# Kernel tuning notes

Hardware: AMD Instinct MI355X
Metric: run time of the kernel (lower is better)

Reference implementation:

```python
import jax, jax.numpy as jnp
import numpy as np

N = 25000; E = 100000; H = 64; NODE_IN = 32; EDGE_IN = 16; L = 3


def _lin(key, fan_in, fan_out):
    kw, kb = jax.random.split(key)
    s = 1.0 / np.sqrt(fan_in)
    W = jax.random.uniform(kw, (fan_out, fan_in), minval=-s, maxval=s, dtype=jnp.float32)
    b = jax.random.uniform(kb, (fan_out,), minval=-s, maxval=s, dtype=jnp.float32)
    return W, b


def setup_inputs() -> dict:
    key = jax.random.key(0)
    ks = jax.random.split(key, 16)
    x = jax.random.normal(ks[0], (N, NODE_IN), dtype=jnp.float32)
    edge_attr = jax.random.normal(ks[1], (E, EDGE_IN), dtype=jnp.float32)
    edge_index = jax.random.randint(ks[2], (2, E), 0, N, dtype=jnp.int32)
    Wn1, bn1 = _lin(ks[3], NODE_IN, H)
    Wn2, bn2 = _lin(ks[4], H, H)
    Wn3, bn3 = _lin(ks[5], H, H)
    We1, be1 = _lin(ks[6], EDGE_IN, H)
    We2, be2 = _lin(ks[7], H, H)
    We3, be3 = _lin(ks[8], H, H * H)
    roots = jax.random.normal(ks[9], (L, H, H), dtype=jnp.float32) / np.sqrt(H)
    conv_bias = jnp.zeros((L, H), dtype=jnp.float32)
    s = 1.0 / np.sqrt(H)
    gru_Wih = jax.random.uniform(ks[10], (3 * H, H), minval=-s, maxval=s, dtype=jnp.float32)
    gru_Whh = jax.random.uniform(ks[11], (3 * H, H), minval=-s, maxval=s, dtype=jnp.float32)
    gru_bih = jax.random.uniform(ks[12], (3 * H,), minval=-s, maxval=s, dtype=jnp.float32)
    gru_bhh = jax.random.uniform(ks[13], (3 * H,), minval=-s, maxval=s, dtype=jnp.float32)
    return dict(x=x, edge_attr=edge_attr,
                Wn1=Wn1, bn1=bn1, Wn2=Wn2, bn2=bn2, Wn3=Wn3, bn3=bn3,
                We1=We1, be1=be1, We2=We2, be2=be2, We3=We3, be3=be3,
                roots=roots, conv_bias=conv_bias,
                gru_Wih=gru_Wih, gru_Whh=gru_Whh, gru_bih=gru_bih, gru_bhh=gru_bhh,
                edge_index=edge_index)


def _mpnn_forward(x, edge_attr, Wn1, bn1, Wn2, bn2, Wn3, bn3,
                  We1, be1, We2, be2, We3, be3,
                  roots, conv_bias, gru_Wih, gru_Whh, gru_bih, gru_bhh, edge_index):
    src, dst = edge_index[0], edge_index[1]
    # mlp_in: Linear-ReLU-Linear-ReLU-Linear
    h = jax.nn.relu(x @ Wn1.T + bn1)
    h = jax.nn.relu(h @ Wn2.T + bn2)
    h = h @ Wn3.T + bn3  # [N, H]
    # edge MLP is shared across all NNConv layers and edge_attr is constant -> compute once
    ew = jax.nn.relu(edge_attr @ We1.T + be1)
    ew = jax.nn.relu(ew @ We2.T + be2)
    ew = (ew @ We3.T + be3).reshape(E, H, H)  # per-edge weight [E, in, out]
    hidden = jnp.zeros((x.shape[0], H), dtype=h.dtype)  # GRU hidden (1 layer)
    for l in range(L):
        # NNConv: message_e = h[src_e] @ W_e, scatter-add to dst, plus root term and bias
        msg = jnp.einsum('ei,eio->eo', h[src], ew)
        aggr = jax.ops.segment_sum(msg, dst, num_segments=N)
        m = aggr + h @ roots[l] + conv_bias[l]  # [N, H]
        # GRU step (seq_len=1, batch=N)
        gi = m @ gru_Wih.T + gru_bih
        gh = hidden @ gru_Whh.T + gru_bhh
        i_r, i_z, i_n = jnp.split(gi, 3, axis=-1)
        h_r, h_z, h_n = jnp.split(gh, 3, axis=-1)
        r = jax.nn.sigmoid(i_r + h_r)
        z = jax.nn.sigmoid(i_z + h_z)
        n = jnp.tanh(i_n + r * h_n)
        hidden = (1.0 - z) * n + z * hidden
        h = hidden  # output of 1-layer GRU == new hidden
    return h


def reference(x, edge_attr, Wn1, bn1, Wn2, bn2, Wn3, bn3,
              We1, be1, We2, be2, We3, be3,
              roots, conv_bias, gru_Wih, gru_Whh, gru_bih, gru_bhh, edge_index):
    return _mpnn_forward(x, edge_attr, Wn1, bn1, Wn2, bn2, Wn3, bn3,
                         We1, be1, We2, be2, We3, be3,
                         roots, conv_bias, gru_Wih, gru_Whh, gru_bih, gru_bhh, edge_index)
```

## Files before the change

### kernel.cpp

```cpp
#include <hip/hip_runtime.h>
#include <math.h>

#define NN 25000
#define NE 100000

typedef _Float16 f16;
typedef _Float16 half8 __attribute__((ext_vector_type(8)));
typedef float f32x4 __attribute__((ext_vector_type(4)));

__global__ __launch_bounds__(256) void prep_all(
    const float* __restrict__ Wn1, const float* __restrict__ Wn2,
    const float* __restrict__ Wn3, const float* __restrict__ We1,
    const float* __restrict__ We2, const float* __restrict__ Wih,
    const float* __restrict__ Whh, const float* __restrict__ We3,
    const float* __restrict__ be3, const float* __restrict__ roots,
    float* __restrict__ T, f16* __restrict__ Wf16, f16* __restrict__ root16,
    f16* __restrict__ Wih16, f16* __restrict__ Whh16)
{
    int f = blockIdx.x * 256 + threadIdx.x;
    if (f >= 318464) return;
    if (f < 15360) {
        if (f < 2048)       { int j = f;         T[f] = Wn1[(j & 63) * 32 + (j >> 6)]; }
        else if (f < 6144)  { int j = f - 2048;  T[f] = Wn2[(j & 63) * 64 + (j >> 6)]; }
        else if (f < 10240) { int j = f - 6144;  T[f] = Wn3[(j & 63) * 64 + (j >> 6)]; }
        else if (f < 11264) { int j = f - 10240; T[f] = We1[(j & 63) * 16 + (j >> 6)]; }
        else                { int j = f - 11264; T[f] = We2[(j & 63) * 64 + (j >> 6)]; }
    } else {
        int g = f - 15360;
        if (g < 266240) {
            if (g < 262144) Wf16[g] = (f16)We3[g];
            else {
                int j = g - 262144; int o = (j >> 6), k = j & 63;
                Wf16[g] = (f16)be3[k * 64 + o];
            }
        } else {
            int g2 = g - 266240;
            if (g2 < 12288) {
                int l = g2 >> 12, j = g2 & 4095, o = j >> 6, i = j & 63;
                root16[g2] = (f16)roots[l * 4096 + i * 64 + o];
            } else if (g2 < 24576) Wih16[g2 - 12288] = (f16)Wih[g2 - 12288];
            else                   Whh16[g2 - 24576] = (f16)Whh[g2 - 24576];
        }
    }
}

__global__ __launch_bounds__(256) void node_mlp(
    const float* __restrict__ x, const float* __restrict__ T,
    const float* __restrict__ bn1, const float* __restrict__ bn2,
    const float* __restrict__ bn3,
    float* __restrict__ hbuf, f16* __restrict__ h16, float* __restrict__ aggr)
{
    __shared__ float sx[4][8][32];
    __shared__ float sh1[4][8][64];
    const float* Wn1T = T;
    const float* Wn2T = T + 2048;
    const float* Wn3T = T + 6144;
    int w = threadIdx.x >> 6, lane = threadIdx.x & 63;
    int n0 = blockIdx.x * 32 + w * 8;
    if (n0 >= NN) return;
    #pragma unroll
    for (int jj = 0; jj < 4; ++jj) {
        int f = jj * 64 + lane;
        sx[w][f >> 5][f & 31] = x[(size_t)(n0 + (f >> 5)) * 32 + (f & 31)];
    }
    float a[8];
    #pragma unroll
    for (int j = 0; j < 8; ++j) a[j] = bn1[lane];
    for (int i = 0; i < 32; i += 4) {
        float4 bb[8];
        #pragma unroll
        for (int j = 0; j < 8; ++j) bb[j] = *(const float4*)&sx[w][j][i];
        #pragma unroll
        for (int ii = 0; ii < 4; ++ii) {
            float wv = Wn1T[(i + ii) * 64 + lane];
            #pragma unroll
            for (int j = 0; j < 8; ++j) a[j] += ((const float*)&bb[j])[ii] * wv;
        }
    }
    #pragma unroll
    for (int j = 0; j < 8; ++j) { sh1[w][j][lane] = fmaxf(a[j], 0.f); a[j] = bn2[lane]; }
    for (int i = 0; i < 64; i += 4) {
        float4 bb[8];
        #pragma unroll
        for (int j = 0; j < 8; ++j) bb[j] = *(const float4*)&sh1[w][j][i];
        #pragma unroll
        for (int ii = 0; ii < 4; ++ii) {
            float wv = Wn2T[(i + ii) * 64 + lane];
            #pragma unroll
            for (int j = 0; j < 8; ++j) a[j] += ((const float*)&bb[j])[ii] * wv;
        }
    }
    #pragma unroll
    for (int j = 0; j < 8; ++j) { sh1[w][j][lane] = fmaxf(a[j], 0.f); a[j] = bn3[lane]; }
    for (int i = 0; i < 64; i += 4) {
        float4 bb[8];
        #pragma unroll
        for (int j = 0; j < 8; ++j) bb[j] = *(const float4*)&sh1[w][j][i];
        #pragma unroll
        for (int ii = 0; ii < 4; ++ii) {
            float wv = Wn3T[(i + ii) * 64 + lane];
            #pragma unroll
            for (int j = 0; j < 8; ++j) a[j] += ((const float*)&bb[j])[ii] * wv;
        }
    }
    #pragma unroll
    for (int j = 0; j < 8; ++j) {
        size_t idx = (size_t)(n0 + j) * 64 + lane;
        hbuf[idx] = a[j];
        h16[idx]  = (f16)a[j];
        aggr[idx] = 0.f;
    }
}

__global__ __launch_bounds__(256) void edge_mlp(
    const float* __restrict__ ea, const float* __restrict__ T,
    const float* __restrict__ be1, const float* __restrict__ be2,
    f16* __restrict__ ew16)
{
    __shared__ float sa[4][8][16];
    __shared__ float st[4][8][64];
    const float* We1T = T + 10240;
    const float* We2T = T + 11264;
    int w = threadIdx.x >> 6, lane = threadIdx.x & 63;
    int e0 = blockIdx.x * 32 + w * 8;
    if (e0 >= NE) return;
    #pragma unroll
    for (int jj = 0; jj < 2; ++jj) {
        int f = jj * 64 + lane;
        sa[w][f >> 4][f & 15] = ea[(size_t)(e0 + (f >> 4)) * 16 + (f & 15)];
    }
    float a[8];
    #pragma unroll
    for (int j = 0; j < 8; ++j) a[j] = be1[lane];
    for (int i = 0; i < 16; i += 4) {
        float4 bb[8];
        #pragma unroll
        for (int j = 0; j < 8; ++j) bb[j] = *(const float4*)&sa[w][j][i];
        #pragma unroll
        for (int ii = 0; ii < 4; ++ii) {
            float wv = We1T[(i + ii) * 64 + lane];
            #pragma unroll
            for (int j = 0; j < 8; ++j) a[j] += ((const float*)&bb[j])[ii] * wv;
        }
    }
    #pragma unroll
    for (int j = 0; j < 8; ++j) { st[w][j][lane] = fmaxf(a[j], 0.f); a[j] = be2[lane]; }
    for (int i = 0; i < 64; i += 4) {
        float4 bb[8];
        #pragma unroll
        for (int j = 0; j < 8; ++j) bb[j] = *(const float4*)&st[w][j][i];
        #pragma unroll
        for (int ii = 0; ii < 4; ++ii) {
            float wv = We2T[(i + ii) * 64 + lane];
            #pragma unroll
            for (int j = 0; j < 8; ++j) a[j] += ((const float*)&bb[j])[ii] * wv;
        }
    }
    #pragma unroll
    for (int j = 0; j < 8; ++j)
        ew16[(size_t)(e0 + j) * 64 + lane] = (f16)fmaxf(a[j], 0.f);
}

__device__ __forceinline__ half8 splat8(f16 v)
{ half8 r = { v, v, v, v, v, v, v, v }; return r; }

__device__ __forceinline__ void mfma_block(
    const char* bb, int swzA, int swzB,
    half8 aA0, half8 aA1, half8 aB0, half8 aB1, f32x4 (&acc)[2][4])
{
    half8 b00 = *(const half8*)(bb + 0    + swzA);
    half8 b01 = *(const half8*)(bb + 0    + swzB);
    half8 b10 = *(const half8*)(bb + 2048 + swzA);
    half8 b11 = *(const half8*)(bb + 2048 + swzB);
    half8 b20 = *(const half8*)(bb + 4096 + swzA);
    half8 b21 = *(const half8*)(bb + 4096 + swzB);
    half8 b30 = *(const half8*)(bb + 6144 + swzA);
    half8 b31 = *(const half8*)(bb + 6144 + swzB);
    acc[0][0] = __builtin_amdgcn_mfma_f32_16x16x32_f16(aA0, b00, acc[0][0], 0, 0, 0);
    acc[0][0] = __builtin_amdgcn_mfma_f32_16x16x32_f16(aA1, b01, acc[0][0], 0, 0, 0);
    acc[0][1] = __builtin_amdgcn_mfma_f32_16x16x32_f16(aA0, b10, acc[0][1], 0, 0, 0);
    acc[0][1] = __builtin_amdgcn_mfma_f32_16x16x32_f16(aA1, b11, acc[0][1], 0, 0, 0);
    acc[0][2] = __builtin_amdgcn_mfma_f32_16x16x32_f16(aA0, b20, acc[0][2], 0, 0, 0);
    acc[0][2] = __builtin_amdgcn_mfma_f32_16x16x32_f16(aA1, b21, acc[0][2], 0, 0, 0);
    acc[0][3] = __builtin_amdgcn_mfma_f32_16x16x32_f16(aA0, b30, acc[0][3], 0, 0, 0);
    acc[0][3] = __builtin_amdgcn_mfma_f32_16x16x32_f16(aA1, b31, acc[0][3], 0, 0, 0);
    acc[1][0] = __builtin_amdgcn_mfma_f32_16x16x32_f16(aB0, b00, acc[1][0], 0, 0, 0);
    acc[1][0] = __builtin_amdgcn_mfma_f32_16x16x32_f16(aB1, b01, acc[1][0], 0, 0, 0);
    acc[1][1] = __builtin_amdgcn_mfma_f32_16x16x32_f16(aB0, b10, acc[1][1], 0, 0, 0);
    acc[1][1] = __builtin_amdgcn_mfma_f32_16x16x32_f16(aB1, b11, acc[1][1], 0, 0, 0);
    acc[1][2] = __builtin_amdgcn_mfma_f32_16x16x32_f16(aB0, b20, acc[1][2], 0, 0, 0);
    acc[1][2] = __builtin_amdgcn_mfma_f32_16x16x32_f16(aB1, b21, acc[1][2], 0, 0, 0);
    acc[1][3] = __builtin_amdgcn_mfma_f32_16x16x32_f16(aB0, b30, acc[1][3], 0, 0, 0);
    acc[1][3] = __builtin_amdgcn_mfma_f32_16x16x32_f16(aB1, b31, acc[1][3], 0, 0, 0);
}

__global__ __launch_bounds__(256) void msg_mfma(
    const f16* __restrict__ h16, const f16* __restrict__ ew16,
    const f16* __restrict__ Wf16, const int* __restrict__ edge_index,
    float* __restrict__ aggr)
{
    __shared__ f16 sh_h[128][72];
    __shared__ f16 sh_ring[4][4096];
    __shared__ int sh_dst[128];
    int t = threadIdx.x, lane = t & 63, wv = t >> 6;
    int e0 = blockIdx.x * 128;
    char* ringc = (char*)&sh_ring[0][0];

    const uint4* gW = (const uint4*)Wf16;
    uint4 r0 = gW[t], r1 = gW[256 + t], r2 = gW[512 + t], r3 = gW[768 + t];

    {
        int row = t >> 1, part = t & 1;
        int e = e0 + row;
        bool valid = e < NE;
        int ec = valid ? e : NE - 1;
        int src = edge_index[ec];
        const uint4* hp = (const uint4*)(h16 + (size_t)src * 64 + part * 32);
        const uint4* ep = (const uint4*)(ew16 + (size_t)ec * 64 + part * 32);
        uint4 z = make_uint4(0u, 0u, 0u, 0u);
        uint4 h0 = hp[0], h1 = hp[1], h2 = hp[2], h3 = hp[3];
        uint4 g0 = valid ? ep[0] : z;
        uint4 g1 = valid ? ep[1] : z;
        uint4 g2 = valid ? ep[2] : z;
        uint4 g3 = valid ? ep[3] : z;
        *(uint4*)&sh_h[row][part * 32]      = h0;
        *(uint4*)&sh_h[row][part * 32 + 8]  = h1;
        *(uint4*)&sh_h[row][part * 32 + 16] = h2;
        *(uint4*)&sh_h[row][part * 32 + 24] = h3;
        int rb = row * 128, key = (row & 7) << 4;
        *(uint4*)(ringc + rb + ((part * 64 +  0) ^ key)) = g0;
        *(uint4*)(ringc + rb + ((part * 64 + 16) ^ key)) = g1;
        *(uint4*)(ringc + rb + ((part * 64 + 32) ^ key)) = g2;
        *(uint4*)(ringc + rb + ((part * 64 + 48) ^ key)) = g3;
        if (lane < 32) {
            int e2 = e0 + wv * 32 + lane;
            sh_dst[wv * 32 + lane] = (e2 < NE) ? edge_index[NE + e2] : -1;
        }
    }

    int r16 = lane & 15, kq = lane >> 4;
    int row0 = wv * 32 + r16, row1 = row0 + 16;

    int k0 = (row0 & 7) << 4, k1 = (row1 & 7) << 4;
    half8 evA0 = *(const half8*)(ringc + row0 * 128 + ((kq * 16) ^ k0));
    half8 evA1 = *(const half8*)(ringc + row0 * 128 + ((64 + kq * 16) ^ k0));
    half8 evB0 = *(const half8*)(ringc + row1 * 128 + ((kq * 16) ^ k1));
    half8 evB1 = *(const half8*)(ringc + row1 * 128 + ((64 + kq * 16) ^ k1));

    __syncthreads();

    int d0 = t * 16, d1 = 4096 + t * 16;
    int dsw0 = d0 ^ (((d0 >> 7) & 7) << 4);
    int dsw1 = d1 ^ (((d1 >> 7) & 7) << 4);

    *(uint4*)(ringc + dsw0) = r0;
    *(uint4*)(ringc + dsw1) = r1;
    *(uint4*)(ringc + 8192 + dsw0) = r2;
    *(uint4*)(ringc + 8192 + dsw1) = r3;
    r0 = gW[2 * 512 + t]; r1 = gW[2 * 512 + 256 + t];
    r2 = gW[3 * 512 + t]; r3 = gW[3 * 512 + 256 + t];
    __syncthreads();

    f32x4 acc[2][4];
    #pragma unroll
    for (int m = 0; m < 2; ++m)
        #pragma unroll
        for (int n = 0; n < 4; ++n) acc[m][n] = (f32x4){0, 0, 0, 0};

    int swzA = (kq << 4) ^ ((r16 & 7) << 4);
    int swzB = ((kq << 4) | 64) ^ ((r16 & 7) << 4);

    for (int i8 = 0; i8 < 8; ++i8) {
        half8 hA = *(const half8*)&sh_h[row0][i8 * 8];
        half8 hB = *(const half8*)&sh_h[row1][i8 * 8];
        #pragma unroll
        for (int w2 = 0; w2 < 4; ++w2) {
            const char* pairR = ringc + (w2 & 1) * 16384 + r16 * 128;
            #pragma unroll
            for (int s = 0; s < 2; ++s) {
                f16 hsA = hA[w2 * 2 + s];
                f16 hsB = hB[w2 * 2 + s];
                mfma_block(pairR + s * 8192, swzA, swzB,
                           evA0 * splat8(hsA), evA1 * splat8(hsA),
                           evB0 * splat8(hsB), evB1 * splat8(hsB), acc);
            }
            char* wb = ringc + ((w2 + 1) & 1) * 16384;
            *(uint4*)(wb + dsw0) = r0;
            *(uint4*)(wb + dsw1) = r1;
            *(uint4*)(wb + 8192 + dsw0) = r2;
            *(uint4*)(wb + 8192 + dsw1) = r3;
            int jw = i8 * 4 + w2;
            int sA = jw * 2 + 4; if (sA > 64) sA = 64;
            int sB = jw * 2 + 5; if (sB > 64) sB = 64;
            r0 = gW[(size_t)sA * 512 + t]; r1 = gW[(size_t)sA * 512 + 256 + t];
            r2 = gW[(size_t)sB * 512 + t]; r3 = gW[(size_t)sB * 512 + 256 + t];
            __syncthreads();
        }
    }

    {
        const char* bb = ringc + r16 * 128;
        half8 aA0 = *(const half8*)&sh_h[row0][kq * 8];
        half8 aA1 = *(const half8*)&sh_h[row0][32 + kq * 8];
        half8 aB0 = *(const half8*)&sh_h[row1][kq * 8];
        half8 aB1 = *(const half8*)&sh_h[row1][32 + kq * 8];
        mfma_block(bb, swzA, swzB, aA0, aA1, aB0, aB1, acc);
    }

    #pragma unroll
    for (int m = 0; m < 2; ++m) {
        #pragma unroll
        for (int reg = 0; reg < 4; ++reg) {
            int e_l = wv * 32 + m * 16 + kq * 4 + reg;
            int d = sh_dst[e_l];
            if (d >= 0) {
                float* ap = aggr + (size_t)d * 64 + r16;
                atomicAdd(ap,      acc[m][0][reg]);
                atomicAdd(ap + 16, acc[m][1][reg]);
                atomicAdd(ap + 32, acc[m][2][reg]);
                atomicAdd(ap + 48, acc[m][3][reg]);
            }
        }
    }
}

__global__ __launch_bounds__(256) void gru_mfma(
    float* __restrict__ aggr, float* __restrict__ hbuf, f16* __restrict__ h16,
    const f16* __restrict__ root16, const float* __restrict__ cbias,
    const f16* __restrict__ Wih16, const f16* __restrict__ Whh16,
    const float* __restrict__ bih, const float* __restrict__ bhh,
    float* __restrict__ out2, int first)
{
    __shared__ f16 sh[64][72];
    __shared__ f16 sm[64][72];
    int t = threadIdx.x, lane = t & 63, wv = t >> 6;
    int n0 = blockIdx.x * 64;

    {
        int row = t >> 2, part = t & 3;
        int n = n0 + row;
        uint4 z = make_uint4(0u, 0u, 0u, 0u);
        const uint4* hp = (const uint4*)(h16 + (size_t)n * 64 + part * 16);
        uint4 v0 = (n < NN) ? hp[0] : z;
        uint4 v1 = (n < NN) ? hp[1] : z;
        *(uint4*)&sh[row][part * 16]     = v0;
        *(uint4*)&sh[row][part * 16 + 8] = v1;
    }
    __syncthreads();

    int r16 = lane & 15, kq = lane >> 4;
    int wr = wv * 16;
    int rowA = wr + r16;
    half8 ah0 = *(const half8*)&sh[rowA][kq * 8];
    half8 ah1 = *(const half8*)&sh[rowA][32 + kq * 8];
    int nodeBase = wr + kq * 4;

    f32x4 accm[4];
    #pragma unroll
    for (int tt = 0; tt < 4; ++tt) {
        int o = tt * 16 + r16;
        float cb = cbias[o];
        #pragma unroll
        for (int reg = 0; reg < 4; ++reg) {
            int n = n0 + nodeBase + reg;
            float v = 0.f;
            if (n < NN) {
                size_t ix = (size_t)n * 64 + o;
                v = aggr[ix] + cb;
                aggr[ix] = 0.f;
            }
            accm[tt][reg] = v;
        }
    }
    #pragma unroll
    for (int tt = 0; tt < 4; ++tt) {
        const f16* bp = root16 + (size_t)(tt * 16 + r16) * 64 + kq * 8;
        half8 b0 = *(const half8*)bp;
        half8 b1 = *(const half8*)(bp + 32);
        accm[tt] = __builtin_amdgcn_mfma_f32_16x16x32_f16(ah0, b0, accm[tt], 0, 0, 0);
        accm[tt] = __builtin_amdgcn_mfma_f32_16x16x32_f16(ah1, b1, accm[tt], 0, 0, 0);
    }
    #pragma unroll
    for (int tt = 0; tt < 4; ++tt)
        #pragma unroll
        for (int reg = 0; reg < 4; ++reg)
            sm[nodeBase + reg][tt * 16 + r16] = (f16)accm[tt][reg];
    __syncthreads();
    half8 am0 = *(const half8*)&sm[rowA][kq * 8];
    half8 am1 = *(const half8*)&sm[rowA][32 + kq * 8];

    f32x4 acc_rz[8], acc_in[4], acc_hn[4];
    #pragma unroll
    for (int tt = 0; tt < 8; ++tt) acc_rz[tt] = (f32x4){0, 0, 0, 0};
    #pragma unroll
    for (int tt = 0; tt < 4; ++tt) { acc_in[tt] = (f32x4){0, 0, 0, 0}; acc_hn[tt] = (f32x4){0, 0, 0, 0}; }

    #pragma unroll
    for (int tt = 0; tt < 8; ++tt) {
        const f16* bp = Wih16 + (size_t)(tt * 16 + r16) * 64 + kq * 8;
        half8 b0 = *(const half8*)bp;
        half8 b1 = *(const half8*)(bp + 32);
        acc_rz[tt] = __builtin_amdgcn_mfma_f32_16x16x32_f16(am0, b0, acc_rz[tt], 0, 0, 0);
        acc_rz[tt] = __builtin_amdgcn_mfma_f32_16x16x32_f16(am1, b1, acc_rz[tt], 0, 0, 0);
    }
    #pragma unroll
    for (int tt = 0; tt < 4; ++tt) {
        const f16* bp = Wih16 + (size_t)(128 + tt * 16 + r16) * 64 + kq * 8;
        half8 b0 = *(const half8*)bp;
        half8 b1 = *(const half8*)(bp + 32);
        acc_in[tt] = __builtin_amdgcn_mfma_f32_16x16x32_f16(am0, b0, acc_in[tt], 0, 0, 0);
        acc_in[tt] = __builtin_amdgcn_mfma_f32_16x16x32_f16(am1, b1, acc_in[tt], 0, 0, 0);
    }
    if (!first) {
        #pragma unroll
        for (int tt = 0; tt < 8; ++tt) {
            const f16* bp = Whh16 + (size_t)(tt * 16 + r16) * 64 + kq * 8;
            half8 b0 = *(const half8*)bp;
            half8 b1 = *(const half8*)(bp + 32);
            acc_rz[tt] = __builtin_amdgcn_mfma_f32_16x16x32_f16(ah0, b0, acc_rz[tt], 0, 0, 0);
            acc_rz[tt] = __builtin_amdgcn_mfma_f32_16x16x32_f16(ah1, b1, acc_rz[tt], 0, 0, 0);
        }
        #pragma unroll
        for (int tt = 0; tt < 4; ++tt) {
            const f16* bp = Whh16 + (size_t)(128 + tt * 16 + r16) * 64 + kq * 8;
            half8 b0 = *(const half8*)bp;
            half8 b1 = *(const half8*)(bp + 32);
            acc_hn[tt] = __builtin_amdgcn_mfma_f32_16x16x32_f16(ah0, b0, acc_hn[tt], 0, 0, 0);
            acc_hn[tt] = __builtin_amdgcn_mfma_f32_16x16x32_f16(ah1, b1, acc_hn[tt], 0, 0, 0);
        }
    }

    #pragma unroll
    for (int tt = 0; tt < 4; ++tt) {
        int o = tt * 16 + r16;
        float b_r = bih[o] + bhh[o];
        float b_z = bih[64 + o] + bhh[64 + o];
        float bin = bih[128 + o];
        float bhn = bhh[128 + o];
        #pragma unroll
        for (int reg = 0; reg < 4; ++reg) {
            int n = n0 + nodeBase + reg;
            if (n >= NN) continue;
            size_t ix = (size_t)n * 64 + o;
            float rv = 1.f / (1.f + expf(-(acc_rz[tt][reg] + b_r)));
            float zv = 1.f / (1.f + expf(-(acc_rz[4 + tt][reg] + b_z)));
            float hn_ = first ? bhn : (acc_hn[tt][reg] + bhn);
            float nv = tanhf(acc_in[tt][reg] + bin + rv * hn_);
            float hold = first ? 0.f : hbuf[ix];
            float outv = (1.f - zv) * nv + zv * hold;
            hbuf[ix] = outv;
            h16[ix]  = (f16)outv;
            if (out2) out2[ix] = outv;
        }
    }
}

extern "C" void kernel_launch(void* const* d_in, const int* in_sizes, int n_in,
                              void* d_out, int out_size, void* d_ws, size_t ws_size,
                              hipStream_t stream)
{
    const float* x   = (const float*)d_in[0];
    const float* ea  = (const float*)d_in[1];
    const float* Wn1 = (const float*)d_in[2];  const float* bn1 = (const float*)d_in[3];
    const float* Wn2 = (const float*)d_in[4];  const float* bn2 = (const float*)d_in[5];
    const float* Wn3 = (const float*)d_in[6];  const float* bn3 = (const float*)d_in[7];
    const float* We1 = (const float*)d_in[8];  const float* be1 = (const float*)d_in[9];
    const float* We2 = (const float*)d_in[10]; const float* be2 = (const float*)d_in[11];
    const float* We3 = (const float*)d_in[12]; const float* be3 = (const float*)d_in[13];
    const float* roots = (const float*)d_in[14];
    const float* cb    = (const float*)d_in[15];
    const float* Wih = (const float*)d_in[16]; const float* Whh = (const float*)d_in[17];
    const float* bih = (const float*)d_in[18]; const float* bhh = (const float*)d_in[19];
    const int*   ei  = (const int*)d_in[20];

    float* ws   = (float*)d_ws;
    float* hbuf = ws;
    float* aggr = hbuf + (size_t)NN * 64;
    float* Tbuf = aggr + (size_t)NN * 64;
    f16*   h16  = (f16*)(ws + 2 * (size_t)NN * 64 + 16384);
    f16*   ew16 = h16  + (size_t)NN * 64;
    f16*   Wf16 = ew16 + (size_t)NE * 64;
    f16*   root16 = Wf16 + 266240;
    f16*   Wih16  = root16 + 12288;
    f16*   Whh16  = Wih16 + 12288;

    prep_all<<<(318464 + 255) / 256, 256, 0, stream>>>(Wn1, Wn2, Wn3, We1, We2,
        Wih, Whh, We3, be3, roots, Tbuf, Wf16, root16, Wih16, Whh16);
    node_mlp<<<(NN + 31) / 32, 256, 0, stream>>>(x, Tbuf, bn1, bn2, bn3,
                                                 hbuf, h16, aggr);
    edge_mlp<<<NE / 32, 256, 0, stream>>>(ea, Tbuf, be1, be2, ew16);

    for (int l = 0; l < 3; ++l) {
        msg_mfma<<<(NE + 127) / 128, 256, 0, stream>>>(h16, ew16, Wf16, ei, aggr);
        gru_mfma<<<(NN + 63) / 64, 256, 0, stream>>>(aggr, hbuf, h16,
            root16 + (size_t)l * 4096, cb + (size_t)l * 64,
            Wih16, Whh16, bih, bhh,
            (l == 2) ? (float*)d_out : nullptr, (l == 0) ? 1 : 0);
    }
}
```

Baseline: 409.4 us.

## Split msg MFMA work by output column per wave; shrink GRU blocks to one wave

The message kernel now assigns each wave a 16-column slice of the output across all 128 edges, instead of 32 edges across all 64 columns. Each B fragment of the per-edge weight is then loaded once and reused across eight M-tiles, which cuts LDS reads per MFMA but holds 16 edge vectors in registers and scales them per tile. It also adds a barrier before the edge loads. The GRU kernel becomes a single-wave 64-thread block over 16 nodes, dropping its __syncthreads; this gives more, smaller blocks and relies on in-wave ordering for the shared-memory exchange.

```diff
diff --git a/kernel.cpp b/kernel.cpp
--- a/kernel.cpp
+++ b/kernel.cpp
@@ -163,36 +163,6 @@
 
 __device__ __forceinline__ half8 splat8(f16 v)
 { half8 r = { v, v, v, v, v, v, v, v }; return r; }
-
-__device__ __forceinline__ void mfma_block(
-    const char* bb, int swzA, int swzB,
-    half8 aA0, half8 aA1, half8 aB0, half8 aB1, f32x4 (&acc)[2][4])
-{
-    half8 b00 = *(const half8*)(bb + 0    + swzA);
-    half8 b01 = *(const half8*)(bb + 0    + swzB);
-    half8 b10 = *(const half8*)(bb + 2048 + swzA);
-    half8 b11 = *(const half8*)(bb + 2048 + swzB);
-    half8 b20 = *(const half8*)(bb + 4096 + swzA);
-    half8 b21 = *(const half8*)(bb + 4096 + swzB);
-    half8 b30 = *(const half8*)(bb + 6144 + swzA);
-    half8 b31 = *(const half8*)(bb + 6144 + swzB);
-    acc[0][0] = __builtin_amdgcn_mfma_f32_16x16x32_f16(aA0, b00, acc[0][0], 0, 0, 0);
-    acc[0][0] = __builtin_amdgcn_mfma_f32_16x16x32_f16(aA1, b01, acc[0][0], 0, 0, 0);
-    acc[0][1] = __builtin_amdgcn_mfma_f32_16x16x32_f16(aA0, b10, acc[0][1], 0, 0, 0);
-    acc[0][1] = __builtin_amdgcn_mfma_f32_16x16x32_f16(aA1, b11, acc[0][1], 0, 0, 0);
-    acc[0][2] = __builtin_amdgcn_mfma_f32_16x16x32_f16(aA0, b20, acc[0][2], 0, 0, 0);
-    acc[0][2] = __builtin_amdgcn_mfma_f32_16x16x32_f16(aA1, b21, acc[0][2], 0, 0, 0);
-    acc[0][3] = __builtin_amdgcn_mfma_f32_16x16x32_f16(aA0, b30, acc[0][3], 0, 0, 0);
-    acc[0][3] = __builtin_amdgcn_mfma_f32_16x16x32_f16(aA1, b31, acc[0][3], 0, 0, 0);
-    acc[1][0] = __builtin_amdgcn_mfma_f32_16x16x32_f16(aB0, b00, acc[1][0], 0, 0, 0);
-    acc[1][0] = __builtin_amdgcn_mfma_f32_16x16x32_f16(aB1, b01, acc[1][0], 0, 0, 0);
-    acc[1][1] = __builtin_amdgcn_mfma_f32_16x16x32_f16(aB0, b10, acc[1][1], 0, 0, 0);
-    acc[1][1] = __builtin_amdgcn_mfma_f32_16x16x32_f16(aB1, b11, acc[1][1], 0, 0, 0);
-    acc[1][2] = __builtin_amdgcn_mfma_f32_16x16x32_f16(aB0, b20, acc[1][2], 0, 0, 0);
-    acc[1][2] = __builtin_amdgcn_mfma_f32_16x16x32_f16(aB1, b21, acc[1][2], 0, 0, 0);
-    acc[1][3] = __builtin_amdgcn_mfma_f32_16x16x32_f16(aB0, b30, acc[1][3], 0, 0, 0);
-    acc[1][3] = __builtin_amdgcn_mfma_f32_16x16x32_f16(aB1, b31, acc[1][3], 0, 0, 0);
-}
 
 __global__ __launch_bounds__(256) void msg_mfma(
     const f16* __restrict__ h16, const f16* __restrict__ ew16,
@@ -237,15 +207,20 @@
             sh_dst[wv * 32 + lane] = (e2 < NE) ? edge_index[NE + e2] : -1;
         }
     }
+    __syncthreads();
 
     int r16 = lane & 15, kq = lane >> 4;
-    int row0 = wv * 32 + r16, row1 = row0 + 16;
-
-    int k0 = (row0 & 7) << 4, k1 = (row1 & 7) << 4;
-    half8 evA0 = *(const half8*)(ringc + row0 * 128 + ((kq * 16) ^ k0));
-    half8 evA1 = *(const half8*)(ringc + row0 * 128 + ((64 + kq * 16) ^ k0));
-    half8 evB0 = *(const half8*)(ringc + row1 * 128 + ((kq * 16) ^ k1));
-    half8 evB1 = *(const half8*)(ringc + row1 * 128 + ((64 + kq * 16) ^ k1));
+
+    half8 ev0[8], ev1[8];
+    {
+        int key = (r16 & 7) << 4;
+        #pragma unroll
+        for (int m = 0; m < 8; ++m) {
+            int row = m * 16 + r16;
+            ev0[m] = *(const half8*)(ringc + row * 128 + ((kq * 16) ^ key));
+            ev1[m] = *(const half8*)(ringc + row * 128 + ((64 + kq * 16) ^ key));
+        }
+    }
 
     __syncthreads();
 
@@ -261,28 +236,35 @@
     r2 = gW[3 * 512 + t]; r3 = gW[3 * 512 + 256 + t];
     __syncthreads();
 
-    f32x4 acc[2][4];
-    #pragma unroll
-    for (int m = 0; m < 2; ++m)
-        #pragma unroll
-        for (int n = 0; n < 4; ++n) acc[m][n] = (f32x4){0, 0, 0, 0};
+    f32x4 acc[8];
+    #pragma unroll
+    for (int m = 0; m < 8; ++m) acc[m] = (f32x4){0, 0, 0, 0};
 
     int swzA = (kq << 4) ^ ((r16 & 7) << 4);
     int swzB = ((kq << 4) | 64) ^ ((r16 & 7) << 4);
+    int colBase = wv * 2048 + r16 * 128;
 
     for (int i8 = 0; i8 < 8; ++i8) {
-        half8 hA = *(const half8*)&sh_h[row0][i8 * 8];
-        half8 hB = *(const half8*)&sh_h[row1][i8 * 8];
+        half8 hM[8];
+        #pragma unroll
+        for (int m = 0; m < 8; ++m)
+            hM[m] = *(const half8*)&sh_h[m * 16 + r16][i8 * 8];
         #pragma unroll
         for (int w2 = 0; w2 < 4; ++w2) {
-            const char* pairR = ringc + (w2 & 1) * 16384 + r16 * 128;
+            const char* pairR = ringc + (w2 & 1) * 16384 + colBase;
             #pragma unroll
             for (int s = 0; s < 2; ++s) {
-                f16 hsA = hA[w2 * 2 + s];
-                f16 hsB = hB[w2 * 2 + s];
-                mfma_block(pairR + s * 8192, swzA, swzB,
-                           evA0 * splat8(hsA), evA1 * splat8(hsA),
-                           evB0 * splat8(hsB), evB1 * splat8(hsB), acc);
+                const char* bb = pairR + s * 8192;
+                half8 bs0 = *(const half8*)(bb + swzA);
+                half8 bs1 = *(const half8*)(bb + swzB);
+                #pragma unroll
+                for (int m = 0; m < 8; ++m) {
+                    f16 hs = hM[m][w2 * 2 + s];
+                    half8 a0 = ev0[m] * splat8(hs);
+                    half8 a1 = ev1[m] * splat8(hs);
+                    acc[m] = __builtin_amdgcn_mfma_f32_16x16x32_f16(a0, bs0, acc[m], 0, 0, 0);
+                    acc[m] = __builtin_amdgcn_mfma_f32_16x16x32_f16(a1, bs1, acc[m], 0, 0, 0);
+                }
             }
             char* wb = ringc + ((w2 + 1) & 1) * 16384;
             *(uint4*)(wb + dsw0) = r0;
@@ -299,45 +281,45 @@
     }
 
     {
-        const char* bb = ringc + r16 * 128;
-        half8 aA0 = *(const half8*)&sh_h[row0][kq * 8];
-        half8 aA1 = *(const half8*)&sh_h[row0][32 + kq * 8];
-        half8 aB0 = *(const half8*)&sh_h[row1][kq * 8];
-        half8 aB1 = *(const half8*)&sh_h[row1][32 + kq * 8];
-        mfma_block(bb, swzA, swzB, aA0, aA1, aB0, aB1, acc);
-    }
-
-    #pragma unroll
-    for (int m = 0; m < 2; ++m) {
+        const char* bb = ringc + colBase;
+        half8 bs0 = *(const half8*)(bb + swzA);
+        half8 bs1 = *(const half8*)(bb + swzB);
+        #pragma unroll
+        for (int m = 0; m < 8; ++m) {
+            int row = m * 16 + r16;
+            half8 a0 = *(const half8*)&sh_h[row][kq * 8];
+            half8 a1 = *(const half8*)&sh_h[row][32 + kq * 8];
+            acc[m] = __builtin_amdgcn_mfma_f32_16x16x32_f16(a0, bs0, acc[m], 0, 0, 0);
+            acc[m] = __builtin_amdgcn_mfma_f32_16x16x32_f16(a1, bs1, acc[m], 0, 0, 0);
+        }
+    }
+
+    #pragma unroll
+    for (int m = 0; m < 8; ++m) {
         #pragma unroll
         for (int reg = 0; reg < 4; ++reg) {
-            int e_l = wv * 32 + m * 16 + kq * 4 + reg;
+            int e_l = m * 16 + kq * 4 + reg;
             int d = sh_dst[e_l];
-            if (d >= 0) {
-                float* ap = aggr + (size_t)d * 64 + r16;
-                atomicAdd(ap,      acc[m][0][reg]);
-                atomicAdd(ap + 16, acc[m][1][reg]);
-                atomicAdd(ap + 32, acc[m][2][reg]);
-                atomicAdd(ap + 48, acc[m][3][reg]);
-            }
-        }
-    }
-}
-
-__global__ __launch_bounds__(256) void gru_mfma(
+            if (d >= 0)
+                atomicAdd(aggr + (size_t)d * 64 + wv * 16 + r16, acc[m][reg]);
+        }
+    }
+}
+
+__global__ __launch_bounds__(64) void gru_mfma(
     float* __restrict__ aggr, float* __restrict__ hbuf, f16* __restrict__ h16,
     const f16* __restrict__ root16, const float* __restrict__ cbias,
     const f16* __restrict__ Wih16, const f16* __restrict__ Whh16,
     const float* __restrict__ bih, const float* __restrict__ bhh,
     float* __restrict__ out2, int first)
 {
-    __shared__ f16 sh[64][72];
-    __shared__ f16 sm[64][72];
-    int t = threadIdx.x, lane = t & 63, wv = t >> 6;
-    int n0 = blockIdx.x * 64;
+    __shared__ f16 sh[16][72];
+    __shared__ f16 sm[16][72];
+    int lane = threadIdx.x & 63;
+    int n0 = blockIdx.x * 16;
 
     {
-        int row = t >> 2, part = t & 3;
+        int row = lane >> 2, part = lane & 3;
         int n = n0 + row;
         uint4 z = make_uint4(0u, 0u, 0u, 0u);
         const uint4* hp = (const uint4*)(h16 + (size_t)n * 64 + part * 16);
@@ -346,14 +328,11 @@
         *(uint4*)&sh[row][part * 16]     = v0;
         *(uint4*)&sh[row][part * 16 + 8] = v1;
     }
-    __syncthreads();
 
     int r16 = lane & 15, kq = lane >> 4;
-    int wr = wv * 16;
-    int rowA = wr + r16;
-    half8 ah0 = *(const half8*)&sh[rowA][kq * 8];
-    half8 ah1 = *(const half8*)&sh[rowA][32 + kq * 8];
-    int nodeBase = wr + kq * 4;
+    half8 ah0 = *(const half8*)&sh[r16][kq * 8];
+    half8 ah1 = *(const half8*)&sh[r16][32 + kq * 8];
+    int nodeBase = kq * 4;
 
     f32x4 accm[4];
     #pragma unroll
@@ -385,9 +364,8 @@
         #pragma unroll
         for (int reg = 0; reg < 4; ++reg)
             sm[nodeBase + reg][tt * 16 + r16] = (f16)accm[tt][reg];
-    __syncthreads();
-    half8 am0 = *(const half8*)&sm[rowA][kq * 8];
-    half8 am1 = *(const half8*)&sm[rowA][32 + kq * 8];
+    half8 am0 = *(const half8*)&sm[r16][kq * 8];
+    half8 am1 = *(const half8*)&sm[r16][32 + kq * 8];
 
     f32x4 acc_rz[8], acc_in[4], acc_hn[4];
     #pragma unroll
@@ -492,7 +470,7 @@
 
     for (int l = 0; l < 3; ++l) {
         msg_mfma<<<(NE + 127) / 128, 256, 0, stream>>>(h16, ew16, Wf16, ei, aggr);
-        gru_mfma<<<(NN + 63) / 64, 256, 0, stream>>>(aggr, hbuf, h16,
+        gru_mfma<<<(NN + 15) / 16, 64, 0, stream>>>(aggr, hbuf, h16,
             root16 + (size_t)l * 4096, cb + (size_t)l * 64,
             Wih16, Whh16, bih, bhh,
             (l == 2) ? (float*)d_out : nullptr, (l == 0) ? 1 : 0);
```

After: 437.1 us. 6.8% more time.
